# Performance work log

Hardware: AMD Instinct MI355X
Metric: run time of the kernel (lower is better)

## Reference

```python
import jax, jax.numpy as jnp
import numpy as np

VOCAB = 50257
EMBED = 256
OUT = 5
B = 512
S = 512

def setup_inputs() -> dict:
    key = jax.random.key(0)
    k1, k2, k3, k4, k5, k6 = jax.random.split(key, 6)
    input_x = jax.random.randint(k1, (B, S), 0, VOCAB, dtype=jnp.int64 if jax.config.jax_enable_x64 else jnp.int32)
    lengths = jax.random.randint(k2, (B,), 1, S + 1, dtype=jnp.int32)  # true ragged lengths in [1, S]
    input_y = jax.random.randint(k3, (B,), 0, OUT, dtype=jnp.int32)
    emb = jax.random.normal(k4, (VOCAB, EMBED), dtype=jnp.float32)
    W = jax.random.normal(k5, (OUT, EMBED), dtype=jnp.float32) * (1.0 / np.sqrt(EMBED))
    b = jax.random.normal(k6, (OUT,), dtype=jnp.float32) * 0.01
    return {"input_x": input_x, "lengths": lengths, "input_y": input_y, "emb": emb, "W": W, "b": b}

def reference(input_x, lengths, input_y, emb, W, b):
    # Embedding gather: [B, S, E]
    x = emb[input_x]
    # Ragged mean pooling via mask (replaces the per-sample Python loop)
    mask = (jnp.arange(S)[None, :] < lengths[:, None]).astype(x.dtype)  # [B, S]
    pooled = jnp.einsum('bse,bs->be', x, mask) / lengths[:, None].astype(x.dtype)  # [B, E]
    # Linear + log-softmax
    logits = pooled @ W.T + b  # [B, O]
    logp = jax.nn.log_softmax(logits, axis=-1)
    # NLLLoss (mean reduction)
    loss = -jnp.take_along_axis(logp, input_y[:, None].astype(jnp.int32), axis=1).mean()
    return loss
```

## Files before the change

### kernel.cpp

```cpp
#include <hip/hip_runtime.h>

#define VOCAB 50257
#define EMBED 256
#define OUT 5
#define BATCH 512
#define SEQ 512
#define PADO 8

__global__ __launch_bounds__(256) void k_embw(const float* __restrict__ emb,
                                              const float* __restrict__ W,
                                              float* __restrict__ embW) {
    const int lane = threadIdx.x & 63;
    const int sub  = lane >> 4;
    const int col  = lane & 15;

    float4 w[OUT][4];
#pragma unroll
    for (int o = 0; o < OUT; ++o)
#pragma unroll
        for (int c = 0; c < 4; ++c)
            w[o][c] = *(const float4*)(W + o * EMBED + col * 16 + c * 4);

    const int waveId = (int)((blockIdx.x * 256u + threadIdx.x) >> 6);
    const int nWaves = (int)gridDim.x * 4;
    const int nQuad  = (VOCAB + 3) / 4;

    for (int q = waveId; q < nQuad; q += nWaves) {
        const int v = q * 4 + sub;
        float p[OUT] = {0.f, 0.f, 0.f, 0.f, 0.f};
        if (v < VOCAB) {
            const float* row = emb + (size_t)v * EMBED + col * 16;
#pragma unroll
            for (int c = 0; c < 4; ++c) {
                const float4 e = *(const float4*)(row + c * 4);
#pragma unroll
                for (int o = 0; o < OUT; ++o)
                    p[o] += e.x * w[o][c].x + e.y * w[o][c].y +
                            e.z * w[o][c].z + e.w * w[o][c].w;
            }
        }
#pragma unroll
        for (int o = 0; o < OUT; ++o) {
#pragma unroll
            for (int off = 8; off > 0; off >>= 1)
                p[o] += __shfl_down(p[o], off, 16);
        }
        if (col == 0 && v < VOCAB) {
            float* dst = embW + (size_t)v * PADO;
            *(float4*)dst = make_float4(p[0], p[1], p[2], p[3]);
            dst[4] = p[4];
        }
    }
}

__global__ __launch_bounds__(256) void k_pool(const int* __restrict__ x,
                                              const int* __restrict__ lengths,
                                              const int* __restrict__ y,
                                              const float* __restrict__ bias,
                                              const float* __restrict__ embW,
                                              float* __restrict__ losses) {
    const int b   = blockIdx.x;
    const int len = lengths[b];
    const int tid = threadIdx.x;

    const int2 tk = ((const int2*)(x + (size_t)b * SEQ))[tid];

    float acc[OUT] = {0.f, 0.f, 0.f, 0.f, 0.f};
    if (2 * tid < len) {
        const float* r = embW + (size_t)tk.x * PADO;
        const float4 a = *(const float4*)r;
        const float a4 = r[4];
        acc[0] += a.x; acc[1] += a.y; acc[2] += a.z; acc[3] += a.w; acc[4] += a4;
    }
    if (2 * tid + 1 < len) {
        const float* r = embW + (size_t)tk.y * PADO;
        const float4 a = *(const float4*)r;
        const float a4 = r[4];
        acc[0] += a.x; acc[1] += a.y; acc[2] += a.z; acc[3] += a.w; acc[4] += a4;
    }

#pragma unroll
    for (int o = 0; o < OUT; ++o) {
#pragma unroll
        for (int off = 32; off > 0; off >>= 1)
            acc[o] += __shfl_down(acc[o], off, 64);
    }

    __shared__ float red[4][OUT];
    const int wave = tid >> 6;
    const int lane = tid & 63;
    if (lane == 0) {
#pragma unroll
        for (int o = 0; o < OUT; ++o) red[wave][o] = acc[o];
    }
    __syncthreads();

    if (tid == 0) {
        float logits[OUT];
        const float inv = 1.0f / (float)len;
#pragma unroll
        for (int o = 0; o < OUT; ++o)
            logits[o] = (red[0][o] + red[1][o] + red[2][o] + red[3][o]) * inv + bias[o];

        float m = logits[0];
#pragma unroll
        for (int o = 1; o < OUT; ++o) m = fmaxf(m, logits[o]);
        float sum = 0.f;
#pragma unroll
        for (int o = 0; o < OUT; ++o) sum += __expf(logits[o] - m);
        const float lse = m + __logf(sum);
        losses[b] = lse - logits[y[b]];
    }
}

__global__ __launch_bounds__(256) void k_reduce(const float* __restrict__ losses,
                                                float* __restrict__ out) {
    float v = losses[threadIdx.x] + losses[threadIdx.x + 256];
#pragma unroll
    for (int off = 32; off > 0; off >>= 1)
        v += __shfl_down(v, off, 64);
    __shared__ float red[4];
    if ((threadIdx.x & 63) == 0) red[threadIdx.x >> 6] = v;
    __syncthreads();
    if (threadIdx.x == 0)
        out[0] = (red[0] + red[1] + red[2] + red[3]) * (1.0f / (float)BATCH);
}

extern "C" void kernel_launch(void* const* d_in, const int* in_sizes, int n_in,
                              void* d_out, int out_size, void* d_ws, size_t ws_size,
                              hipStream_t stream) {
    const int*   x       = (const int*)d_in[0];
    const int*   lengths = (const int*)d_in[1];
    const int*   y       = (const int*)d_in[2];
    const float* emb     = (const float*)d_in[3];
    const float* W       = (const float*)d_in[4];
    const float* bias    = (const float*)d_in[5];

    float* embW   = (float*)d_ws;
    float* losses = embW + (size_t)VOCAB * PADO;

    k_embw<<<1024, 256, 0, stream>>>(emb, W, embW);
    k_pool<<<BATCH, 256, 0, stream>>>(x, lengths, y, bias, embW, losses);
    k_reduce<<<1, 256, 0, stream>>>(losses, (float*)d_out);
}
```

Measured before the change: 101.5 us.

## Fuse three kernels into one persistent kernel with atomic grid barriers

Merges the vocab projection, per-sample pooling/loss, and final mean into a single 512-block kernel. Global atomic counters act as grid-wide barriers between the stages, and a memset resets them before each launch. This removes two kernel launch gaps. In exchange, the projection stage now runs on half as many blocks, spin-waiting adds latency, and the barrier relies on all 512 blocks being co-resident.

```diff
diff --git a/kernel.cpp b/kernel.cpp
--- a/kernel.cpp
+++ b/kernel.cpp
@@ -6,124 +6,151 @@
 #define BATCH 512
 #define SEQ 512
 #define PADO 8
+#define NBLK 512
 
-__global__ __launch_bounds__(256) void k_embw(const float* __restrict__ emb,
-                                              const float* __restrict__ W,
-                                              float* __restrict__ embW) {
-    const int lane = threadIdx.x & 63;
+__global__ __launch_bounds__(256) void k_fused(const int* __restrict__ x,
+                                               const int* __restrict__ lengths,
+                                               const int* __restrict__ y,
+                                               const float* __restrict__ emb,
+                                               const float* __restrict__ W,
+                                               const float* __restrict__ bias,
+                                               unsigned* __restrict__ cnt,
+                                               float* __restrict__ embW,
+                                               float* __restrict__ losses,
+                                               float* __restrict__ out) {
+    __shared__ float red[4][OUT];
+    __shared__ float red2[4];
+
+    const int tid  = threadIdx.x;
+    const int lane = tid & 63;
     const int sub  = lane >> 4;
     const int col  = lane & 15;
 
-    float4 w[OUT][4];
+    {
+        float4 w[OUT][4];
 #pragma unroll
-    for (int o = 0; o < OUT; ++o)
+        for (int o = 0; o < OUT; ++o)
 #pragma unroll
-        for (int c = 0; c < 4; ++c)
-            w[o][c] = *(const float4*)(W + o * EMBED + col * 16 + c * 4);
+            for (int c = 0; c < 4; ++c)
+                w[o][c] = *(const float4*)(W + o * EMBED + col * 16 + c * 4);
 
-    const int waveId = (int)((blockIdx.x * 256u + threadIdx.x) >> 6);
-    const int nWaves = (int)gridDim.x * 4;
-    const int nQuad  = (VOCAB + 3) / 4;
+        const int waveId = (int)((blockIdx.x * 256u + tid) >> 6);
+        const int nWaves = NBLK * 4;
+        const int nQuad  = (VOCAB + 3) / 4;
 
-    for (int q = waveId; q < nQuad; q += nWaves) {
-        const int v = q * 4 + sub;
-        float p[OUT] = {0.f, 0.f, 0.f, 0.f, 0.f};
-        if (v < VOCAB) {
-            const float* row = emb + (size_t)v * EMBED + col * 16;
+        for (int q = waveId; q < nQuad; q += nWaves) {
+            const int v = q * 4 + sub;
+            float p[OUT] = {0.f, 0.f, 0.f, 0.f, 0.f};
+            if (v < VOCAB) {
+                const float* row = emb + (size_t)v * EMBED + col * 16;
 #pragma unroll
-            for (int c = 0; c < 4; ++c) {
-                const float4 e = *(const float4*)(row + c * 4);
+                for (int c = 0; c < 4; ++c) {
+                    const float4 e = *(const float4*)(row + c * 4);
 #pragma unroll
-                for (int o = 0; o < OUT; ++o)
-                    p[o] += e.x * w[o][c].x + e.y * w[o][c].y +
-                            e.z * w[o][c].z + e.w * w[o][c].w;
+                    for (int o = 0; o < OUT; ++o)
+                        p[o] += e.x * w[o][c].x + e.y * w[o][c].y +
+                                e.z * w[o][c].z + e.w * w[o][c].w;
+                }
+            }
+#pragma unroll
+            for (int o = 0; o < OUT; ++o) {
+#pragma unroll
+                for (int off = 8; off > 0; off >>= 1)
+                    p[o] += __shfl_down(p[o], off, 16);
+            }
+            if (col == 0 && v < VOCAB) {
+                float* dst = embW + (size_t)v * PADO;
+                *(float4*)dst = make_float4(p[0], p[1], p[2], p[3]);
+                dst[4] = p[4];
             }
         }
+    }
+
+    __syncthreads();
+    if (tid == 0) {
+        __threadfence();
+        __hip_atomic_fetch_add(&cnt[0], 1u, __ATOMIC_RELEASE,
+                               __HIP_MEMORY_SCOPE_AGENT);
+        while (__hip_atomic_load(&cnt[0], __ATOMIC_ACQUIRE,
+                                 __HIP_MEMORY_SCOPE_AGENT) < (unsigned)NBLK) {
+            __builtin_amdgcn_s_sleep(1);
+        }
+    }
+    __syncthreads();
+
+    {
+        const int b   = blockIdx.x;
+        const int len = lengths[b];
+
+        const int2 tk = ((const int2*)(x + (size_t)b * SEQ))[tid];
+
+        float acc[OUT] = {0.f, 0.f, 0.f, 0.f, 0.f};
+        if (2 * tid < len) {
+            const float* r = embW + (size_t)tk.x * PADO;
+            const float4 a = *(const float4*)r;
+            const float a4 = r[4];
+            acc[0] += a.x; acc[1] += a.y; acc[2] += a.z; acc[3] += a.w; acc[4] += a4;
+        }
+        if (2 * tid + 1 < len) {
+            const float* r = embW + (size_t)tk.y * PADO;
+            const float4 a = *(const float4*)r;
+            const float a4 = r[4];
+            acc[0] += a.x; acc[1] += a.y; acc[2] += a.z; acc[3] += a.w; acc[4] += a4;
+        }
+
 #pragma unroll
         for (int o = 0; o < OUT; ++o) {
 #pragma unroll
-            for (int off = 8; off > 0; off >>= 1)
-                p[o] += __shfl_down(p[o], off, 16);
+            for (int off = 32; off > 0; off >>= 1)
+                acc[o] += __shfl_down(acc[o], off, 64);
         }
-        if (col == 0 && v < VOCAB) {
-            float* dst = embW + (size_t)v * PADO;
-            *(float4*)dst = make_float4(p[0], p[1], p[2], p[3]);
-            dst[4] = p[4];
+
+        const int wave = tid >> 6;
+        if ((tid & 63) == 0) {
+#pragma unroll
+            for (int o = 0; o < OUT; ++o) red[wave][o] = acc[o];
+        }
+        __syncthreads();
+
+        if (tid == 0) {
+            float logits[OUT];
+            const float inv = 1.0f / (float)len;
+#pragma unroll
+            for (int o = 0; o < OUT; ++o)
+                logits[o] = (red[0][o] + red[1][o] + red[2][o] + red[3][o]) * inv + bias[o];
+
+            float m = logits[0];
+#pragma unroll
+            for (int o = 1; o < OUT; ++o) m = fmaxf(m, logits[o]);
+            float sum = 0.f;
+#pragma unroll
+            for (int o = 0; o < OUT; ++o) sum += __expf(logits[o] - m);
+            const float lse = m + __logf(sum);
+            losses[b] = lse - logits[y[b]];
+
+            __hip_atomic_fetch_add(&cnt[1], 1u, __ATOMIC_RELEASE,
+                                   __HIP_MEMORY_SCOPE_AGENT);
         }
     }
-}
 
-__global__ __launch_bounds__(256) void k_pool(const int* __restrict__ x,
-                                              const int* __restrict__ lengths,
-                                              const int* __restrict__ y,
-                                              const float* __restrict__ bias,
-                                              const float* __restrict__ embW,
-                                              float* __restrict__ losses) {
-    const int b   = blockIdx.x;
-    const int len = lengths[b];
-    const int tid = threadIdx.x;
+    if (blockIdx.x != 0) return;
 
-    const int2 tk = ((const int2*)(x + (size_t)b * SEQ))[tid];
-
-    float acc[OUT] = {0.f, 0.f, 0.f, 0.f, 0.f};
-    if (2 * tid < len) {
-        const float* r = embW + (size_t)tk.x * PADO;
-        const float4 a = *(const float4*)r;
-        const float a4 = r[4];
-        acc[0] += a.x; acc[1] += a.y; acc[2] += a.z; acc[3] += a.w; acc[4] += a4;
-    }
-    if (2 * tid + 1 < len) {
-        const float* r = embW + (size_t)tk.y * PADO;
-        const float4 a = *(const float4*)r;
-        const float a4 = r[4];
-        acc[0] += a.x; acc[1] += a.y; acc[2] += a.z; acc[3] += a.w; acc[4] += a4;
-    }
-
-#pragma unroll
-    for (int o = 0; o < OUT; ++o) {
-#pragma unroll
-        for (int off = 32; off > 0; off >>= 1)
-            acc[o] += __shfl_down(acc[o], off, 64);
-    }
-
-    __shared__ float red[4][OUT];
-    const int wave = tid >> 6;
-    const int lane = tid & 63;
-    if (lane == 0) {
-#pragma unroll
-        for (int o = 0; o < OUT; ++o) red[wave][o] = acc[o];
+    if (tid == 0) {
+        while (__hip_atomic_load(&cnt[1], __ATOMIC_ACQUIRE,
+                                 __HIP_MEMORY_SCOPE_AGENT) < (unsigned)NBLK) {
+            __builtin_amdgcn_s_sleep(1);
+        }
     }
     __syncthreads();
 
-    if (tid == 0) {
-        float logits[OUT];
-        const float inv = 1.0f / (float)len;
-#pragma unroll
-        for (int o = 0; o < OUT; ++o)
-            logits[o] = (red[0][o] + red[1][o] + red[2][o] + red[3][o]) * inv + bias[o];
-
-        float m = logits[0];
-#pragma unroll
-        for (int o = 1; o < OUT; ++o) m = fmaxf(m, logits[o]);
-        float sum = 0.f;
-#pragma unroll
-        for (int o = 0; o < OUT; ++o) sum += __expf(logits[o] - m);
-        const float lse = m + __logf(sum);
-        losses[b] = lse - logits[y[b]];
-    }
-}
-
-__global__ __launch_bounds__(256) void k_reduce(const float* __restrict__ losses,
-                                                float* __restrict__ out) {
-    float v = losses[threadIdx.x] + losses[threadIdx.x + 256];
+    float v = losses[tid] + losses[tid + 256];
 #pragma unroll
     for (int off = 32; off > 0; off >>= 1)
         v += __shfl_down(v, off, 64);
-    __shared__ float red[4];
-    if ((threadIdx.x & 63) == 0) red[threadIdx.x >> 6] = v;
+    if ((tid & 63) == 0) red2[tid >> 6] = v;
     __syncthreads();
-    if (threadIdx.x == 0)
-        out[0] = (red[0] + red[1] + red[2] + red[3]) * (1.0f / (float)BATCH);
+    if (tid == 0)
+        out[0] = (red2[0] + red2[1] + red2[2] + red2[3]) * (1.0f / (float)BATCH);
 }
 
 extern "C" void kernel_launch(void* const* d_in, const int* in_sizes, int n_in,
@@ -136,10 +163,13 @@
     const float* W       = (const float*)d_in[4];
     const float* bias    = (const float*)d_in[5];
 
-    float* embW   = (float*)d_ws;
-    float* losses = embW + (size_t)VOCAB * PADO;
+    unsigned* cnt    = (unsigned*)d_ws;
+    float*    embW   = (float*)((char*)d_ws + 256);
+    float*    losses = embW + (size_t)VOCAB * PADO;
+    float*    outp   = (float*)d_out;
 
-    k_embw<<<1024, 256, 0, stream>>>(emb, W, embW);
-    k_pool<<<BATCH, 256, 0, stream>>>(x, lengths, y, bias, embW, losses);
-    k_reduce<<<1, 256, 0, stream>>>(losses, (float*)d_out);
+    hipMemsetAsync(cnt, 0, 2 * sizeof(unsigned), stream);
+
+    k_fused<<<NBLK, 256, 0, stream>>>(x, lengths, y, emb, W, bias, cnt, embW,
+                                      losses, outp);
 }
```

After: 159.5 us. 57.2% more time.
